# Kernel optimization log

Measured on AMD Instinct MI355X. Metric: run time of the kernel, lower is better.

Reference implementation:

```python
import jax, jax.numpy as jnp
from jax import lax
import numpy as np

INPUT_POINTS = 4096
NUM_STAGES = 4
EMBED_DIM = 72
K_NEIGHBORS = 90
ALPHA = 1000.0
BETA = 100.0
B = 4
EPS = 1e-5


def pos_embed(coords, out_dim):
    """coords: [B, Cin, *rest] -> [B, out_dim, *rest].
    Matches PosE_Initial/PosE_Geo: sin/cos interleaved along the feature axis."""
    Bsz, cin = coords.shape[0], coords.shape[1]
    rest = coords.shape[2:]
    feat_dim = out_dim // (cin * 2)
    dim_embed = ALPHA ** (jnp.arange(feat_dim, dtype=coords.dtype) / feat_dim)
    div = BETA * coords[..., None] / dim_embed                 # [B,Cin,*rest,f]
    emb = jnp.stack([jnp.sin(div), jnp.cos(div)], axis=-1)      # [B,Cin,*rest,f,2]
    emb = emb.reshape(coords.shape + (2 * feat_dim,))           # interleave sin/cos
    emb = jnp.moveaxis(emb, -1, 2)                              # [B,Cin,2f,*rest]
    return emb.reshape((Bsz, out_dim) + rest)


def fps(points, n):
    """Farthest point sampling, deterministic start at index 0. points [N,3]."""
    d0 = jnp.full(points.shape[0], jnp.inf, dtype=points.dtype)

    def step(carry, _):
        d, last = carry
        dist = jnp.sum((points - points[last]) ** 2, axis=-1)
        d = jnp.minimum(d, dist)
        return (d, jnp.argmax(d)), last

    _, idx = lax.scan(step, (d0, jnp.argmax(jnp.zeros(points.shape[0]))), None, length=n)
    return idx


def gather_points(points, idx):
    # points [B,N,C], idx [B,...] -> [B,...,C]
    return jax.vmap(lambda p, i: p[i])(points, idx)


def knn_indices(xyz, new_xyz, k):
    # squared pairwise distances [B,S,N] then k smallest
    sq = (jnp.sum(new_xyz ** 2, -1)[:, :, None]
          + jnp.sum(xyz ** 2, -1)[:, None, :]
          - 2.0 * jnp.einsum('bsc,bnc->bsn', new_xyz, xyz))
    _, idx = lax.top_k(-sq, k)
    return idx


def stage(xyz, x, group_num, out_dim, gamma, beta_p):
    # xyz [B,N,3], x [B,N,C]
    fi = fps(xyz[0], group_num)                 # shared across batch (fps with batch=None)
    lc_xyz = xyz[:, fi]                         # [B,G,3]
    lc_x = x[:, fi]                             # [B,G,C]
    ki = knn_indices(xyz, lc_xyz, K_NEIGHBORS)  # [B,G,K]
    knn_xyz = gather_points(xyz, ki)            # [B,G,K,3]
    knn_x = gather_points(x, ki)                # [B,G,K,C]
    # LGA: global scalar std (unbiased, like torch.std) normalization
    dx = knn_x - lc_x[:, :, None, :]
    dxyz = knn_xyz - lc_xyz[:, :, None, :]
    knn_xn = dx / (jnp.std(dx, ddof=1) + EPS)
    knn_xyzn = dxyz / (jnp.std(dxyz, ddof=1) + EPS)
    feat = jnp.concatenate(
        [knn_xn, jnp.broadcast_to(lc_x[:, :, None, :], knn_xn.shape)], axis=-1)
    feat = jnp.transpose(feat, (0, 3, 1, 2))                    # [B,out,G,K]
    pe = pos_embed(jnp.transpose(knn_xyzn, (0, 3, 1, 2)), out_dim)
    w = (feat + pe) * pe                                        # [B,out,G,K]
    # Pooling: max+mean over K, BatchNorm1d (training stats), exact GELU
    lc = jnp.max(w, -1) + jnp.mean(w, -1)                       # [B,out,G]
    mu = jnp.mean(lc, axis=(0, 2), keepdims=True)
    var = jnp.var(lc, axis=(0, 2), keepdims=True)
    lc = (lc - mu) / jnp.sqrt(var + EPS) * gamma[None, :, None] + beta_p[None, :, None]
    return lc_xyz, jax.nn.gelu(lc, approximate=False)


def forward(xyz, x, gammas, betas):
    feat = pos_embed(x, EMBED_DIM)              # [B,72,N]
    out_dim = EMBED_DIM
    group = INPUT_POINTS
    for i in range(NUM_STAGES):
        out_dim *= 2
        group //= 2
        xyz, feat = stage(xyz, jnp.transpose(feat, (0, 2, 1)),
                          group, out_dim, gammas[i], betas[i])
    return jnp.max(feat, -1) + jnp.mean(feat, -1)


def setup_inputs() -> dict:
    key = jax.random.key(0)
    k1, k2 = jax.random.split(key)
    inp = {
        'xyz': jax.random.normal(k1, (B, INPUT_POINTS, 3), jnp.float32),
        'x': jax.random.normal(k2, (B, 3, INPUT_POINTS), jnp.float32),
    }
    dims = [EMBED_DIM * 2 ** (i + 1) for i in range(NUM_STAGES)]
    for i, d in enumerate(dims):
        inp[f'gamma{i}'] = jnp.ones((d,), jnp.float32)
        inp[f'beta{i}'] = jnp.zeros((d,), jnp.float32)
    return inp


def reference(xyz, x, gamma0, beta0, gamma1, beta1, gamma2, beta2, gamma3, beta3):
    return forward(xyz, x,
                   [gamma0, gamma1, gamma2, gamma3],
                   [beta0, beta1, beta2, beta3])
```

## Files before the change

kernel.cpp:

```cpp
#include <hip/hip_runtime.h>

typedef unsigned int u32;
typedef unsigned long long u64;
typedef float v2f __attribute__((ext_vector_type(2)));

#define BB 4
#define NP0 4096
#define KNB 90
#define CC0 72
#define MAXD 1152
#define NSTRIPE 16
#define FSPLIT 850

__global__ void k_init(const float* __restrict__ xyz, const float* __restrict__ x,
                       float* __restrict__ xs, float* __restrict__ ys, float* __restrict__ zs,
                       float* __restrict__ feat, float* __restrict__ sums){
  int i = blockIdx.x*blockDim.x + threadIdx.x;
  if (i < 16) sums[i] = 0.f;
  if (i < BB*NP0){
    xs[i] = xyz[3*i+0];
    ys[i] = xyz[3*i+1];
    zs[i] = xyz[3*i+2];
  }
  if (i < BB*NP0*36){
    int j = i % 36; int bn = i / 36;
    int n = bn % NP0, b = bn / NP0;
    int cin = j / 12, f = j % 12;
    float xv = x[(b*3+cin)*NP0 + n];
    float rcp = __powf(1000.0f, -(float)f / 12.0f);
    float a = (100.0f * xv) * rcp;
    float sn, cs; __sincosf(a, &sn, &cs);
    float2 v = make_float2(sn, cs);
    *(float2*)(feat + (size_t)bn*CC0 + cin*24 + 2*f) = v;
  }
}

__device__ __forceinline__ void wave_argmax(float bd, int bi, float &smax, int &wbi){
  float v = bd;
  #define DPP_MAX(ctrl) do{ int _t = __builtin_amdgcn_mov_dpp(__float_as_int(v), (ctrl), 0xf, 0xf, true); \
                            v = fmaxf(v, __int_as_float(_t)); }while(0)
  DPP_MAX(0x111); DPP_MAX(0x112); DPP_MAX(0x114); DPP_MAX(0x118);
  DPP_MAX(0x142); DPP_MAX(0x143);
  #undef DPP_MAX
  smax = __int_as_float(__builtin_amdgcn_readlane(__float_as_int(v), 63));
  u64 msk = __ballot(bd == smax);
  int winlane = (int)__ffsll((long long)msk) - 1;
  wbi = __builtin_amdgcn_readlane(bi, winlane);
}

template<int PPT>
__global__ __launch_bounds__(256)
void k_fps4(const float* __restrict__ xs, const float* __restrict__ ys, const float* __restrict__ zs,
            int N, int G, int* __restrict__ fi,
            float* __restrict__ nxs, float* __restrict__ nys, float* __restrict__ nzs){
  constexpr int PH = PPT/2;
  __shared__ float4 sp[4096];
  __shared__ int sfi[2048];
  __shared__ u64 cand[2][4];
  int tid = threadIdx.x;
  const int base = tid * PPT;
  int wv = tid >> 6;
  int lane = tid & 63;
  v2f px[PH], py[PH], pz[PH], dmn[PH];
  #pragma unroll
  for (int j=0;j<PH;j++){
    int n = base + 2*j;
    float2 ax = *(const float2*)(xs+n);
    float2 ay = *(const float2*)(ys+n);
    float2 az = *(const float2*)(zs+n);
    px[j] = (v2f){ax.x, ax.y};
    py[j] = (v2f){ay.x, ay.y};
    pz[j] = (v2f){az.x, az.y};
    sp[n]   = make_float4(ax.x, ay.x, az.x, 0.f);
    sp[n+1] = make_float4(ax.y, ay.y, az.y, 0.f);
    dmn[j] = (v2f){INFINITY, INFINITY};
  }
  if (tid==0){ sfi[0]=0; }
  float lx = xs[0], ly = ys[0], lz = zs[0];
  __syncthreads();
  for (int t=1; t<G; t++){
    float bd = -INFINITY; int bi = base;
    v2f lx2 = (v2f){lx,lx}, ly2 = (v2f){ly,ly}, lz2 = (v2f){lz,lz};
    {
      #pragma clang fp contract(off)
      #pragma unroll
      for (int j=0;j<PH;j++){
        v2f dx = px[j] - lx2;
        v2f dy = py[j] - ly2;
        v2f dz = pz[j] - lz2;
        v2f d2 = (dx*dx + dy*dy) + dz*dz;
        v2f dmo = dmn[j];
        float dm0 = fminf(dmo.x, d2.x);
        float dm1 = fminf(dmo.y, d2.y);
        dmn[j] = (v2f){dm0, dm1};
        bool g0 = dm0 > bd;
        bd = g0 ? dm0 : bd;
        bi = g0 ? (base + 2*j) : bi;
        bool g1 = dm1 > bd;
        bd = g1 ? dm1 : bd;
        bi = g1 ? (base + 2*j + 1) : bi;
      }
    }
    float smax; int wbi;
    wave_argmax(bd, bi, smax, wbi);
    int par = t & 1;
    if (lane == 0) cand[par][wv] = ((u64)__float_as_uint(smax) << 32) | (u32)(~(u32)wbi);
    __syncthreads();
    u64 k0 = cand[par][0], k1 = cand[par][1], k2 = cand[par][2], k3 = cand[par][3];
    u64 ka = k0 > k1 ? k0 : k1;
    u64 kb = k2 > k3 ? k2 : k3;
    u64 km = ka > kb ? ka : kb;
    int w = (int)(~(u32)km);
    if ((u32)w >= (u32)N) w = 0;
    float4 p = sp[w];
    lx = p.x; ly = p.y; lz = p.z;
    if (tid==0){ sfi[t] = w; }
  }
  __syncthreads();
  for (int i = tid; i < G; i += 256) fi[i] = sfi[i];
  for (int i = tid; i < BB*G; i += 256){
    int b = i / G, g = i % G;
    int idx = sfi[g];
    nxs[i] = xs[(size_t)b*N + idx];
    nys[i] = ys[(size_t)b*N + idx];
    nzs[i] = zs[(size_t)b*N + idx];
  }
}

template<int NF, int NT, bool LDSST>
__device__ __forceinline__
void fps_chunk(const float* __restrict__ cxs, const float* __restrict__ cys, const float* __restrict__ czs,
               int t0, int t1,
               float* __restrict__ dmnG, float4* __restrict__ cenG,
               int* __restrict__ fi2,
               float* __restrict__ n2xs, float* __restrict__ n2ys, float* __restrict__ n2zs,
               u64 (&cand)[2][4], float4* __restrict__ sp){
  constexpr int PPT = NF/NT;
  constexpr int PH = PPT/2;
  constexpr int G2 = NF/2;
  constexpr int NW = NT/64;
  int tid = threadIdx.x;
  const int base = tid * PPT;
  int wv = tid >> 6, lane = tid & 63;
  v2f px[PH], py[PH], pz[PH], dmn[PH];
  #pragma unroll
  for (int j=0;j<PH;j++){
    int n = base + 2*j;
    float2 ax = *(const float2*)(cxs+n);
    float2 ay = *(const float2*)(cys+n);
    float2 az = *(const float2*)(czs+n);
    px[j] = (v2f){ax.x, ax.y};
    py[j] = (v2f){ay.x, ay.y};
    pz[j] = (v2f){az.x, az.y};
    if constexpr (LDSST){
      sp[n]   = make_float4(ax.x, ay.x, az.x, 0.f);
      sp[n+1] = make_float4(ax.y, ay.y, az.y, 0.f);
    }
  }
  float lx, ly, lz;
  if (t0 == 1){
    #pragma unroll
    for (int j=0;j<PH;j++) dmn[j] = (v2f){INFINITY, INFINITY};
    if (tid==0) fi2[0] = 0;
    lx = cxs[0]; ly = cys[0]; lz = czs[0];
  } else {
    #pragma unroll
    for (int j=0;j<PH;j++){
      float2 dv = *(const float2*)(dmnG + base + 2*j);
      dmn[j] = (v2f){dv.x, dv.y};
    }
    float4 c = *cenG;
    lx = c.x; ly = c.y; lz = c.z;
  }
  __syncthreads();
  for (int t=t0; t<t1; t++){
    float bd = -INFINITY; int bi = base;
    v2f lx2 = (v2f){lx,lx}, ly2 = (v2f){ly,ly}, lz2 = (v2f){lz,lz};
    {
      #pragma clang fp contract(off)
      #pragma unroll
      for (int j=0;j<PH;j++){
        v2f dx = px[j] - lx2;
        v2f dy = py[j] - ly2;
        v2f dz = pz[j] - lz2;
        v2f d2 = (dx*dx + dy*dy) + dz*dz;
        v2f dmo = dmn[j];
        float dm0 = fminf(dmo.x, d2.x);
        float dm1 = fminf(dmo.y, d2.y);
        dmn[j] = (v2f){dm0, dm1};
        bool g0 = dm0 > bd;
        bd = g0 ? dm0 : bd;
        bi = g0 ? (base + 2*j) : bi;
        bool g1 = dm1 > bd;
        bd = g1 ? dm1 : bd;
        bi = g1 ? (base + 2*j + 1) : bi;
      }
    }
    float smax; int wbi;
    wave_argmax(bd, bi, smax, wbi);
    int par = t & 1;
    if (lane == 0) cand[par][wv] = ((u64)__float_as_uint(smax) << 32) | (u32)(~(u32)wbi);
    __syncthreads();
    u64 km;
    if constexpr (NW >= 4){
      u64 k0 = cand[par][0], k1 = cand[par][1], k2 = cand[par][2], k3 = cand[par][3];
      u64 ka = k0 > k1 ? k0 : k1;
      u64 kb = k2 > k3 ? k2 : k3;
      km = ka > kb ? ka : kb;
    } else {
      u64 k0 = cand[par][0], k1 = cand[par][1];
      km = k0 > k1 ? k0 : k1;
    }
    int w = (int)(~(u32)km);
    if ((u32)w >= (u32)NF) w = 0;
    if constexpr (LDSST){
      float4 p = sp[w];
      lx = p.x; ly = p.y; lz = p.z;
    } else {
      lx = cxs[w]; ly = cys[w]; lz = czs[w];
    }
    if (tid==0) fi2[t] = w;
  }
  if (t1 < G2){
    #pragma unroll
    for (int j=0;j<PH;j++)
      *(float2*)(dmnG + base + 2*j) = make_float2(dmn[j].x, dmn[j].y);
    if (tid==0) *cenG = make_float4(lx, ly, lz, 0.f);
  } else {
    __syncthreads();
    for (int i = tid; i < BB*G2; i += NT){
      int b2 = i / G2, g2 = i % G2;
      int idx = fi2[g2];
      if ((u32)idx >= (u32)NF) idx = 0;
      n2xs[i] = cxs[(size_t)b2*NF + idx];
      n2ys[i] = cys[(size_t)b2*NF + idx];
      n2zs[i] = czs[(size_t)b2*NF + idx];
    }
  }
}

__device__ float blockReduceSum(float v, float* sRed){
  for (int off=32; off; off>>=1) v += __shfl_down(v, off, 64);
  int wid = threadIdx.x >> 6, lane = threadIdx.x & 63;
  __syncthreads();
  if (lane==0) sRed[wid] = v;
  __syncthreads();
  float r = 0;
  if (threadIdx.x == 0){ for (int i=0;i<4;i++) r += sRed[i]; }
  return r;
}

template<int C, int NF>
__global__ __launch_bounds__(256)
void k_knnstd(const float* __restrict__ x,
              const float* __restrict__ xs, const float* __restrict__ ys, const float* __restrict__ zs,
              const float* __restrict__ nxs, const float* __restrict__ nys, const float* __restrict__ nzs,
              const int* __restrict__ fi, int N, int G,
              int* __restrict__ ki, float* __restrict__ sums,
              int t0, int t1, float* __restrict__ dmnG, float4* __restrict__ cenG,
              int* __restrict__ fi2, float* __restrict__ n2xs,
              float* __restrict__ n2ys, float* __restrict__ n2zs){
  extern __shared__ u32 smk[];
  __shared__ u64 candF[2][4];
  int tid = threadIdx.x;
  if constexpr (NF > 0){
    if (blockIdx.x == 0){
      fps_chunk<NF,256,true>(nxs, nys, nzs, t0, t1, dmnG, cenG, fi2, n2xs, n2ys, n2zs, candF, (float4*)smk);
      return;
    }
  }
  u32* keys = smk;
  u32* hist = smk + N;
  u32* eq   = hist + 256;
  u32* sc   = eq + 512;
  u32* wtot = sc + 4;
  __shared__ float sLcx[C];
  __shared__ int sKi[KNB];
  __shared__ int sFi;
  __shared__ float sRed[4];
  int bid = (NF > 0) ? ((int)blockIdx.x - 1) : (int)blockIdx.x;
  int wv = tid >> 6, lane = tid & 63;
  int g = bid % G, b = bid / G;
  if (tid==0){ int f0 = fi[g]; if ((u32)f0 >= (u32)N) f0 = 0; sFi = f0; }
  float cx = nxs[b*G+g], cy = nys[b*G+g], cz = nzs[b*G+g];
  float ss = __fadd_rn(__fadd_rn(__fmul_rn(cx,cx), __fmul_rn(cy,cy)), __fmul_rn(cz,cz));
  for (int n = tid; n < N; n += 256){
    float px = xs[b*N+n], py = ys[b*N+n], pz = zs[b*N+n];
    float nn  = __fadd_rn(__fadd_rn(__fmul_rn(px,px), __fmul_rn(py,py)), __fmul_rn(pz,pz));
    float dot = __fadd_rn(__fadd_rn(__fmul_rn(cx,px), __fmul_rn(cy,py)), __fmul_rn(cz,pz));
    float sq  = __fsub_rn(__fadd_rn(ss, nn), __fmul_rn(2.0f, dot));
    u32 u = __float_as_uint(sq);
    keys[n] = (u & 0x80000000u) ? ~u : (u | 0x80000000u);
  }
  if (tid < 4) sc[tid] = 0;
  __syncthreads();
  for (int c = tid; c < C; c += 256) sLcx[c] = x[(size_t)(b*N + sFi)*C + c];
  u32 prefix = 0, bas = 0;
  for (int pass=0; pass<4; pass++){
    int shift = 24 - 8*pass;
    u32 mask = (pass==0) ? 0u : (0xFFFFFFFFu << (shift+8));
    hist[tid] = 0;
    __syncthreads();
    for (int n = tid; n < N; n += 256){
      u32 k = keys[n];
      if ((k & mask) == (prefix & mask))
        atomicAdd(&hist[(k >> shift) & 255u], 1u);
    }
    __syncthreads();
    u32 h = hist[tid];
    u32 p = h;
    #pragma unroll
    for (int off=1; off<64; off<<=1){
      u32 o = __shfl_up(p, off, 64);
      if (lane >= off) p += o;
    }
    if (lane == 63) wtot[wv] = p;
    __syncthreads();
    u32 ex = p - h;
    for (int w2=0; w2<wv; w2++) ex += wtot[w2];
    if (bas + ex < KNB && bas + ex + h >= KNB){
      sc[0] = prefix | ((u32)tid << shift);
      sc[1] = bas + ex;
    }
    __syncthreads();
    prefix = sc[0]; bas = sc[1];
    __syncthreads();
  }
  u32 T = prefix;
  int needEq = KNB - (int)bas;
  int* out = ki + (size_t)(b*G+g)*KNB;
  for (int n = tid; n < N; n += 256){
    u32 k = keys[n];
    if (k < T){
      u32 p2 = atomicAdd(&sc[2], 1u);
      if (p2 < KNB){ out[p2] = n; sKi[p2] = n; }
    } else if (k == T){
      u32 e = atomicAdd(&sc[3], 1u);
      if (e < 512) eq[e] = (u32)n;
    }
  }
  __syncthreads();
  int m = (int)sc[3]; if (m > 512) m = 512;
  for (int i = tid; i < m; i += 256){
    u32 v = eq[i];
    int r = 0;
    for (int j=0; j<m; j++) r += (eq[j] < v);
    if (r < needEq){
      u32 p2 = atomicAdd(&sc[2], 1u);
      if (p2 < KNB){ out[p2] = (int)v; sKi[p2] = (int)v; }
    }
  }
  __syncthreads();
  if (tid == 0){
    u32 c = sc[2];
    while (c < KNB){ out[c] = 0; sKi[c] = 0; c++; }
  }
  __syncthreads();
  float s1=0, s2=0, s3=0, s4=0;
  constexpr int C2 = C/2;
  for (int u2 = tid; u2 < KNB*C2; u2 += 256){
    int k = u2 / C2; int c = (u2 - k*C2)*2;
    int idx = sKi[k];
    float2 v = *(const float2*)(x + (size_t)(b*N + idx)*C + c);
    float a0 = v.x - sLcx[c];
    float a1 = v.y - sLcx[c+1];
    s1 += a0 + a1; s2 += a0*a0 + a1*a1;
  }
  if (tid < 3){
    for (int k=0;k<KNB;k++){
      int idx = sKi[k];
      float pc = (tid==0 ? xs[b*N+idx] : tid==1 ? ys[b*N+idx] : zs[b*N+idx]);
      float cc = (tid==0 ? cx : tid==1 ? cy : cz);
      float w = pc - cc;
      s3 += w; s4 += w*w;
    }
  }
  float t;
  t = blockReduceSum(s1, sRed); if (tid==0) atomicAdd(&sums[0], t);
  t = blockReduceSum(s2, sRed); if (tid==0) atomicAdd(&sums[1], t);
  t = blockReduceSum(s3, sRed); if (tid==0) atomicAdd(&sums[2], t);
  t = blockReduceSum(s4, sRed); if (tid==0) atomicAdd(&sums[3], t);
}

template<int C, int NF, int NT>
__global__ void k_feat(const float* __restrict__ x,
            const float* __restrict__ xs, const float* __restrict__ ys, const float* __restrict__ zs,
            const float* __restrict__ nxs, const float* __restrict__ nys, const float* __restrict__ nzs,
            const int* __restrict__ fi, const int* __restrict__ ki, const float* __restrict__ sums,
            double n1, double n2,
            int N, int G, float* __restrict__ lc,
            int t0, int t1, float* __restrict__ dmnG, float4* __restrict__ cenG,
            int* __restrict__ fi2, float* __restrict__ n2xs,
            float* __restrict__ n2ys, float* __restrict__ n2zs){
  constexpr int D = 2*C;
  constexpr int D3 = D/3;
  constexpr int FD = C/3;
  __shared__ u64 candF[2][4];
  __shared__ float sLcx[C];
  __shared__ float sDx[KNB*3];
  __shared__ int sKi[KNB];
  __shared__ int sFi;
  __shared__ float sC[3];
  __shared__ float sInv2[2];
  int tid = threadIdx.x;
  if constexpr (NF > 0){
    if (blockIdx.x == 0){
      fps_chunk<NF,NT,false>(nxs, nys, nzs, t0, t1, dmnG, cenG, fi2, n2xs, n2ys, n2zs, candF, nullptr);
      return;
    }
  }
  int bid = (NF > 0) ? ((int)blockIdx.x - 1) : (int)blockIdx.x;
  int g = bid % G, b = bid / G;
  if (tid==0){ int f0 = fi[g]; if ((u32)f0 >= (u32)N) f0 = 0; sFi = f0; }
  if (tid==0){
    double s1 = sums[0], s2 = sums[1];
    double mean = s1/n1;
    double var = (s2 - s1*mean)/(n1 - 1.0); if (var < 0) var = 0;
    sInv2[0] = (float)(1.0/(sqrt(var) + 1e-5));
    double t1d = sums[2], t2d = sums[3];
    double m2 = t1d/n2;
    double v2 = (t2d - t1d*m2)/(n2 - 1.0); if (v2 < 0) v2 = 0;
    sInv2[1] = (float)(1.0/(sqrt(v2) + 1e-5));
  }
  if (tid<3) sC[tid] = (tid==0 ? nxs[b*G+g] : tid==1 ? nys[b*G+g] : nzs[b*G+g]);
  if (tid < KNB){ int v = ki[(size_t)(b*G+g)*KNB + tid]; if ((u32)v >= (u32)N) v = 0; sKi[tid] = v; }
  __syncthreads();
  for (int c = tid; c < C; c += blockDim.x) sLcx[c] = x[(size_t)(b*N + sFi)*C + c];
  for (int t = tid; t < KNB*3; t += blockDim.x){
    int k = t/3, c = t%3;
    int idx = sKi[k];
    float pc = (c==0 ? xs[b*N+idx] : c==1 ? ys[b*N+idx] : zs[b*N+idx]);
    sDx[t] = (pc - sC[c]) * sInv2[1];
  }
  __syncthreads();
  int p = tid;
  if (p >= C) return;
  int d0 = 2*p;
  int c = d0 / D3;
  int f = (d0 - c*D3) >> 1;
  float rcp = __powf(1000.0f, -(float)f / (float)FD);
  bool low = (d0 < C);
  float invdx = sInv2[0];
  float fh0 = 0.f, fh1 = 0.f;
  if (!low){ fh0 = sLcx[d0-C]; fh1 = sLcx[d0+1-C]; }
  float l0 = low ? sLcx[d0] : 0.f, l1 = low ? sLcx[d0+1] : 0.f;
  float mx0=-INFINITY, mx1=-INFINITY, sm0=0.f, sm1=0.f;
  for (int k=0;k<KNB;k++){
    float a = (100.0f * sDx[k*3+c]) * rcp;
    float sn, cs; __sincosf(a, &sn, &cs);
    float f0, f1;
    if (low){
      float2 v = *(const float2*)(x + (size_t)(b*N + sKi[k])*C + d0);
      f0 = (v.x - l0) * invdx;
      f1 = (v.y - l1) * invdx;
    } else { f0 = fh0; f1 = fh1; }
    float w0 = (f0 + sn)*sn;
    float w1 = (f1 + cs)*cs;
    mx0 = fmaxf(mx0, w0); sm0 += w0;
    mx1 = fmaxf(mx1, w1); sm1 += w1;
  }
  float* o = lc + (size_t)(b*G+g)*D + d0;
  o[0] = mx0 + sm0/90.0f;
  o[1] = mx1 + sm1/90.0f;
}

__global__ __launch_bounds__(256)
void k_bnpart(const float* __restrict__ lc, int D, int M,
              double* __restrict__ PS, double* __restrict__ PQ){
  __shared__ double sS[4][64], sQ[4][64];
  int lane = threadIdx.x & 63, row = threadIdx.x >> 6;
  int tile = blockIdx.x, stripe = blockIdx.y;
  int d = tile*64 + lane;
  int span = M / NSTRIPE;
  int i0 = stripe * span;
  double s=0, q=0;
  if (d < D){
    for (int i=i0+row; i<i0+span; i+=4){
      float v = lc[(size_t)i*D + d];
      s += v; q += (double)v*v;
    }
  }
  sS[row][lane]=s; sQ[row][lane]=q;
  __syncthreads();
  if (row==0 && d < D){
    PS[(size_t)stripe*MAXD + d] = sS[0][lane]+sS[1][lane]+sS[2][lane]+sS[3][lane];
    PQ[(size_t)stripe*MAXD + d] = sQ[0][lane]+sQ[1][lane]+sQ[2][lane]+sQ[3][lane];
  }
}

__global__ void k_bnfin(const double* __restrict__ PS, const double* __restrict__ PQ,
                        const float* __restrict__ gamma, const float* __restrict__ beta,
                        int D, int M, float* __restrict__ A, float* __restrict__ Bb){
  int d = blockIdx.x*64 + threadIdx.x;
  if (d >= D) return;
  double ts=0, tq=0;
  for (int s=0; s<NSTRIPE; s++){ ts += PS[(size_t)s*MAXD + d]; tq += PQ[(size_t)s*MAXD + d]; }
  double mean = ts / M;
  double var = tq / M - mean*mean; if (var < 0) var = 0;
  float rstd = (float)(1.0/sqrt(var + 1e-5));
  float gm = gamma[d], bt = beta[d];
  A[d] = gm*rstd;
  Bb[d] = bt - (float)mean*gm*rstd;
}

__global__ void k_apply(float* __restrict__ lc, const float* __restrict__ A,
                        const float* __restrict__ Bb, int D, int total){
  int i = blockIdx.x*blockDim.x + threadIdx.x;
  if (i >= total) return;
  int d = i % D;
  float v = lc[i]*A[d] + Bb[d];
  lc[i] = 0.5f * v * (1.0f + erff(v * 0.70710678118654752f));
}

__global__ void k_out(const float* __restrict__ feat, float* __restrict__ out){
  int i = blockIdx.x*blockDim.x + threadIdx.x;
  if (i >= BB*1152) return;
  int b = i / 1152, d = i % 1152;
  const float* base = feat + (size_t)b*256*1152 + d;
  float mx = -INFINITY, sm = 0.f;
  for (int g=0; g<256; g++){
    float v = base[(size_t)g*1152];
    mx = fmaxf(mx, v); sm += v;
  }
  out[i] = mx + sm/256.0f;
}

extern "C" void kernel_launch(void* const* d_in, const int* in_sizes, int n_in,
                              void* d_out, int out_size, void* d_ws, size_t ws_size,
                              hipStream_t stream) {
  const float* xyz = (const float*)d_in[0];
  const float* xin = (const float*)d_in[1];
  float* ws = (float*)d_ws;
  size_t off = 0;
  const size_t PS_ = (size_t)BB*NP0;
  const size_t XS = (size_t)BB*NP0*CC0;
  float* T0[3]; float* T1[3]; float* T2[3];
  for (int i=0;i<3;i++){ T0[i] = ws + off; off += PS_; }
  for (int i=0;i<3;i++){ T1[i] = ws + off; off += PS_; }
  for (int i=0;i<3;i++){ T2[i] = ws + off; off += PS_; }
  float* xA = ws + off; off += XS;
  float* xB = ws + off; off += XS;
  int*   fiA = (int*)(ws + off); off += 2048;
  int*   fiB = (int*)(ws + off); off += 2048;
  int*   ki = (int*)(ws + off); off += (size_t)BB*2048*KNB;
  float* sums = ws + off; off += 16;
  float* Abn  = ws + off; off += 1152;
  float* Bbn  = ws + off; off += 1152;
  float* dmnG = ws + off; off += 2048;
  float4* cenG = (float4*)(ws + off); off += 4;
  off = (off + 1) & ~(size_t)1;
  double* PSb = (double*)(ws + off); off += (size_t)NSTRIPE*MAXD*2;
  double* PQb = (double*)(ws + off); off += (size_t)NSTRIPE*MAXD*2;

  k_init<<<(BB*NP0*36+255)/256, 256, 0, stream>>>(xyz, xin, T0[0], T0[1], T0[2], xA, sums);
  k_fps4<16><<<1, 256, 0, stream>>>(T0[0],T0[1],T0[2], NP0, NP0/2, fiA, T1[0],T1[1],T1[2]);

  float **P = T0, **Cn = T1, **Nx = T2;
  int *fiC = fiA, *fiN = fiB;
  float *xc = xA, *lc = xB;
  for (int s=0; s<4; s++){
    int N = NP0 >> s, G = N >> 1, C = CC0 << s, D = 2*C;
    float* ssum = sums + 4*s;
    size_t knn_need = (size_t)(N + 256 + 512 + 8 + 8)*4;
    if (s==0){
      size_t lds = knn_need; size_t fps_need = (size_t)2048*16;
      if (fps_need > lds) lds = fps_need;
      k_knnstd<72,2048><<<BB*G+1, 256, lds, stream>>>(xc, P[0],P[1],P[2], Cn[0],Cn[1],Cn[2],
          fiC, N, G, ki, ssum, 1, FSPLIT, dmnG, cenG, fiN, Nx[0],Nx[1],Nx[2]);
    } else if (s==1){
      size_t lds = knn_need; size_t fps_need = (size_t)1024*16;
      if (fps_need > lds) lds = fps_need;
      k_knnstd<144,1024><<<BB*G+1, 256, lds, stream>>>(xc, P[0],P[1],P[2], Cn[0],Cn[1],Cn[2],
          fiC, N, G, ki, ssum, 1, 512, dmnG, cenG, fiN, Nx[0],Nx[1],Nx[2]);
    } else if (s==2){
      size_t lds = knn_need; size_t fps_need = (size_t)512*16;
      if (fps_need > lds) lds = fps_need;
      k_knnstd<288,512><<<BB*G+1, 256, lds, stream>>>(xc, P[0],P[1],P[2], Cn[0],Cn[1],Cn[2],
          fiC, N, G, ki, ssum, 1, 256, dmnG, cenG, fiN, Nx[0],Nx[1],Nx[2]);
    } else {
      k_knnstd<576,0><<<BB*G, 256, knn_need, stream>>>(xc, P[0],P[1],P[2], Cn[0],Cn[1],Cn[2],
          fiC, N, G, ki, ssum, 0, 0, nullptr, nullptr, nullptr, nullptr, nullptr, nullptr);
    }
    double n1 = (double)BB*G*KNB*C, n2 = (double)BB*G*KNB*3;
    int Tp = ((C + 63)/64)*64;
    if (s==0){
      k_feat<72,2048,128><<<BB*G+1, Tp, 0, stream>>>(xc, P[0],P[1],P[2], Cn[0],Cn[1],Cn[2], fiC, ki, ssum,
          n1, n2, N, G, lc, FSPLIT, 1024, dmnG, cenG, fiN, Nx[0],Nx[1],Nx[2]);
    } else if (s==1){
      k_feat<144,0,0><<<BB*G, Tp, 0, stream>>>(xc, P[0],P[1],P[2], Cn[0],Cn[1],Cn[2], fiC, ki, ssum,
          n1, n2, N, G, lc, 0, 0, nullptr, nullptr, nullptr, nullptr, nullptr, nullptr);
    } else if (s==2){
      k_feat<288,0,0><<<BB*G, Tp, 0, stream>>>(xc, P[0],P[1],P[2], Cn[0],Cn[1],Cn[2], fiC, ki, ssum,
          n1, n2, N, G, lc, 0, 0, nullptr, nullptr, nullptr, nullptr, nullptr, nullptr);
    } else {
      k_feat<576,0,0><<<BB*G, Tp, 0, stream>>>(xc, P[0],P[1],P[2], Cn[0],Cn[1],Cn[2], fiC, ki, ssum,
          n1, n2, N, G, lc, 0, 0, nullptr, nullptr, nullptr, nullptr, nullptr, nullptr);
    }
    int M = BB*G;
    dim3 bng((D + 63)/64, NSTRIPE);
    k_bnpart<<<bng, 256, 0, stream>>>(lc, D, M, PSb, PQb);
    k_bnfin<<<(D + 63)/64, 64, 0, stream>>>(PSb, PQb, (const float*)d_in[2+2*s],
                                            (const float*)d_in[3+2*s], D, M, Abn, Bbn);
    int total = M*D;
    k_apply<<<(total+255)/256, 256, 0, stream>>>(lc, Abn, Bbn, D, total);
    float** t = P; P = Cn; Cn = Nx; Nx = t;
    int* ti = fiC; fiC = fiN; fiN = ti;
    float* tf = xc; xc = lc; lc = tf;
  }
  k_out<<<(BB*1152+255)/256, 256, 0, stream>>>(xc, (float*)d_out);
}
```

Baseline: 2.531 ms.

## Run FPS inside the KNN kernel and let KNN blocks spin on per-index flags

Result: no change. 2.572 ms (+1.6%).

```diff
diff --git a/kernel.cpp b/kernel.cpp
--- a/kernel.cpp
+++ b/kernel.cpp
@@ -10,13 +10,29 @@
 #define CC0 72
 #define MAXD 1152
 #define NSTRIPE 16
-#define FSPLIT 850
+#define T1S 300
+#define T2S 200
+
+__device__ __forceinline__ void fi_store(int* p, int v){
+  __hip_atomic_store(p, v, __ATOMIC_RELAXED, __HIP_MEMORY_SCOPE_AGENT);
+}
+__device__ __forceinline__ int fi_spin(const int* p){
+  int v = __hip_atomic_load((int*)p, __ATOMIC_RELAXED, __HIP_MEMORY_SCOPE_AGENT);
+  int guard = 0;
+  while (v == -1 && guard < (1<<20)){
+    __builtin_amdgcn_s_sleep(8);
+    v = __hip_atomic_load((int*)p, __ATOMIC_RELAXED, __HIP_MEMORY_SCOPE_AGENT);
+    guard++;
+  }
+  return v;
+}
 
 __global__ void k_init(const float* __restrict__ xyz, const float* __restrict__ x,
                        float* __restrict__ xs, float* __restrict__ ys, float* __restrict__ zs,
-                       float* __restrict__ feat, float* __restrict__ sums){
+                       float* __restrict__ feat, float* __restrict__ sums, int* __restrict__ fiALL){
   int i = blockIdx.x*blockDim.x + threadIdx.x;
   if (i < 16) sums[i] = 0.f;
+  if (i < 3840) fiALL[i] = -1;
   if (i < BB*NP0){
     xs[i] = xyz[3*i+0];
     ys[i] = xyz[3*i+1];
@@ -46,85 +62,6 @@
   u64 msk = __ballot(bd == smax);
   int winlane = (int)__ffsll((long long)msk) - 1;
   wbi = __builtin_amdgcn_readlane(bi, winlane);
-}
-
-template<int PPT>
-__global__ __launch_bounds__(256)
-void k_fps4(const float* __restrict__ xs, const float* __restrict__ ys, const float* __restrict__ zs,
-            int N, int G, int* __restrict__ fi,
-            float* __restrict__ nxs, float* __restrict__ nys, float* __restrict__ nzs){
-  constexpr int PH = PPT/2;
-  __shared__ float4 sp[4096];
-  __shared__ int sfi[2048];
-  __shared__ u64 cand[2][4];
-  int tid = threadIdx.x;
-  const int base = tid * PPT;
-  int wv = tid >> 6;
-  int lane = tid & 63;
-  v2f px[PH], py[PH], pz[PH], dmn[PH];
-  #pragma unroll
-  for (int j=0;j<PH;j++){
-    int n = base + 2*j;
-    float2 ax = *(const float2*)(xs+n);
-    float2 ay = *(const float2*)(ys+n);
-    float2 az = *(const float2*)(zs+n);
-    px[j] = (v2f){ax.x, ax.y};
-    py[j] = (v2f){ay.x, ay.y};
-    pz[j] = (v2f){az.x, az.y};
-    sp[n]   = make_float4(ax.x, ay.x, az.x, 0.f);
-    sp[n+1] = make_float4(ax.y, ay.y, az.y, 0.f);
-    dmn[j] = (v2f){INFINITY, INFINITY};
-  }
-  if (tid==0){ sfi[0]=0; }
-  float lx = xs[0], ly = ys[0], lz = zs[0];
-  __syncthreads();
-  for (int t=1; t<G; t++){
-    float bd = -INFINITY; int bi = base;
-    v2f lx2 = (v2f){lx,lx}, ly2 = (v2f){ly,ly}, lz2 = (v2f){lz,lz};
-    {
-      #pragma clang fp contract(off)
-      #pragma unroll
-      for (int j=0;j<PH;j++){
-        v2f dx = px[j] - lx2;
-        v2f dy = py[j] - ly2;
-        v2f dz = pz[j] - lz2;
-        v2f d2 = (dx*dx + dy*dy) + dz*dz;
-        v2f dmo = dmn[j];
-        float dm0 = fminf(dmo.x, d2.x);
-        float dm1 = fminf(dmo.y, d2.y);
-        dmn[j] = (v2f){dm0, dm1};
-        bool g0 = dm0 > bd;
-        bd = g0 ? dm0 : bd;
-        bi = g0 ? (base + 2*j) : bi;
-        bool g1 = dm1 > bd;
-        bd = g1 ? dm1 : bd;
-        bi = g1 ? (base + 2*j + 1) : bi;
-      }
-    }
-    float smax; int wbi;
-    wave_argmax(bd, bi, smax, wbi);
-    int par = t & 1;
-    if (lane == 0) cand[par][wv] = ((u64)__float_as_uint(smax) << 32) | (u32)(~(u32)wbi);
-    __syncthreads();
-    u64 k0 = cand[par][0], k1 = cand[par][1], k2 = cand[par][2], k3 = cand[par][3];
-    u64 ka = k0 > k1 ? k0 : k1;
-    u64 kb = k2 > k3 ? k2 : k3;
-    u64 km = ka > kb ? ka : kb;
-    int w = (int)(~(u32)km);
-    if ((u32)w >= (u32)N) w = 0;
-    float4 p = sp[w];
-    lx = p.x; ly = p.y; lz = p.z;
-    if (tid==0){ sfi[t] = w; }
-  }
-  __syncthreads();
-  for (int i = tid; i < G; i += 256) fi[i] = sfi[i];
-  for (int i = tid; i < BB*G; i += 256){
-    int b = i / G, g = i % G;
-    int idx = sfi[g];
-    nxs[i] = xs[(size_t)b*N + idx];
-    nys[i] = ys[(size_t)b*N + idx];
-    nzs[i] = zs[(size_t)b*N + idx];
-  }
 }
 
 template<int NF, int NT, bool LDSST>
@@ -140,95 +77,104 @@
   constexpr int G2 = NF/2;
   constexpr int NW = NT/64;
   int tid = threadIdx.x;
+  const bool act = (tid < NT);
   const int base = tid * PPT;
   int wv = tid >> 6, lane = tid & 63;
   v2f px[PH], py[PH], pz[PH], dmn[PH];
-  #pragma unroll
-  for (int j=0;j<PH;j++){
-    int n = base + 2*j;
-    float2 ax = *(const float2*)(cxs+n);
-    float2 ay = *(const float2*)(cys+n);
-    float2 az = *(const float2*)(czs+n);
-    px[j] = (v2f){ax.x, ax.y};
-    py[j] = (v2f){ay.x, ay.y};
-    pz[j] = (v2f){az.x, az.y};
-    if constexpr (LDSST){
-      sp[n]   = make_float4(ax.x, ay.x, az.x, 0.f);
-      sp[n+1] = make_float4(ax.y, ay.y, az.y, 0.f);
-    }
-  }
-  float lx, ly, lz;
-  if (t0 == 1){
-    #pragma unroll
-    for (int j=0;j<PH;j++) dmn[j] = (v2f){INFINITY, INFINITY};
-    if (tid==0) fi2[0] = 0;
-    lx = cxs[0]; ly = cys[0]; lz = czs[0];
-  } else {
+  float lx=0.f, ly=0.f, lz=0.f;
+  if (act){
     #pragma unroll
     for (int j=0;j<PH;j++){
-      float2 dv = *(const float2*)(dmnG + base + 2*j);
-      dmn[j] = (v2f){dv.x, dv.y};
-    }
-    float4 c = *cenG;
-    lx = c.x; ly = c.y; lz = c.z;
+      int n = base + 2*j;
+      float2 ax = *(const float2*)(cxs+n);
+      float2 ay = *(const float2*)(cys+n);
+      float2 az = *(const float2*)(czs+n);
+      px[j] = (v2f){ax.x, ax.y};
+      py[j] = (v2f){ay.x, ay.y};
+      pz[j] = (v2f){az.x, az.y};
+      if constexpr (LDSST){
+        sp[n]   = make_float4(ax.x, ay.x, az.x, 0.f);
+        sp[n+1] = make_float4(ax.y, ay.y, az.y, 0.f);
+      }
+    }
+    if (t0 == 1){
+      #pragma unroll
+      for (int j=0;j<PH;j++) dmn[j] = (v2f){INFINITY, INFINITY};
+      if (tid==0) fi_store(&fi2[0], 0);
+      lx = cxs[0]; ly = cys[0]; lz = czs[0];
+    } else {
+      #pragma unroll
+      for (int j=0;j<PH;j++){
+        float2 dv = *(const float2*)(dmnG + base + 2*j);
+        dmn[j] = (v2f){dv.x, dv.y};
+      }
+      float4 c = *cenG;
+      lx = c.x; ly = c.y; lz = c.z;
+    }
   }
   __syncthreads();
   for (int t=t0; t<t1; t++){
     float bd = -INFINITY; int bi = base;
-    v2f lx2 = (v2f){lx,lx}, ly2 = (v2f){ly,ly}, lz2 = (v2f){lz,lz};
-    {
-      #pragma clang fp contract(off)
+    float smax; int wbi;
+    if (act){
+      v2f lx2 = (v2f){lx,lx}, ly2 = (v2f){ly,ly}, lz2 = (v2f){lz,lz};
+      {
+        #pragma clang fp contract(off)
+        #pragma unroll
+        for (int j=0;j<PH;j++){
+          v2f dx = px[j] - lx2;
+          v2f dy = py[j] - ly2;
+          v2f dz = pz[j] - lz2;
+          v2f d2 = (dx*dx + dy*dy) + dz*dz;
+          v2f dmo = dmn[j];
+          float dm0 = fminf(dmo.x, d2.x);
+          float dm1 = fminf(dmo.y, d2.y);
+          dmn[j] = (v2f){dm0, dm1};
+          bool g0 = dm0 > bd;
+          bd = g0 ? dm0 : bd;
+          bi = g0 ? (base + 2*j) : bi;
+          bool g1 = dm1 > bd;
+          bd = g1 ? dm1 : bd;
+          bi = g1 ? (base + 2*j + 1) : bi;
+        }
+      }
+      wave_argmax(bd, bi, smax, wbi);
+      if (lane == 0) cand[t & 1][wv] = ((u64)__float_as_uint(smax) << 32) | (u32)(~(u32)wbi);
+    }
+    __syncthreads();
+    if (act){
+      int par = t & 1;
+      u64 km;
+      if constexpr (NW >= 4){
+        u64 k0 = cand[par][0], k1 = cand[par][1], k2 = cand[par][2], k3 = cand[par][3];
+        u64 ka = k0 > k1 ? k0 : k1;
+        u64 kb = k2 > k3 ? k2 : k3;
+        km = ka > kb ? ka : kb;
+      } else {
+        u64 k0 = cand[par][0], k1 = cand[par][1];
+        km = k0 > k1 ? k0 : k1;
+      }
+      int w = (int)(~(u32)km);
+      if ((u32)w >= (u32)NF) w = 0;
+      if constexpr (LDSST){
+        float4 p = sp[w];
+        lx = p.x; ly = p.y; lz = p.z;
+      } else {
+        lx = cxs[w]; ly = cys[w]; lz = czs[w];
+      }
+      if (tid==0) fi_store(&fi2[t], w);
+    }
+  }
+  if (t1 < G2){
+    if (act){
       #pragma unroll
-      for (int j=0;j<PH;j++){
-        v2f dx = px[j] - lx2;
-        v2f dy = py[j] - ly2;
-        v2f dz = pz[j] - lz2;
-        v2f d2 = (dx*dx + dy*dy) + dz*dz;
-        v2f dmo = dmn[j];
-        float dm0 = fminf(dmo.x, d2.x);
-        float dm1 = fminf(dmo.y, d2.y);
-        dmn[j] = (v2f){dm0, dm1};
-        bool g0 = dm0 > bd;
-        bd = g0 ? dm0 : bd;
-        bi = g0 ? (base + 2*j) : bi;
-        bool g1 = dm1 > bd;
-        bd = g1 ? dm1 : bd;
-        bi = g1 ? (base + 2*j + 1) : bi;
-      }
-    }
-    float smax; int wbi;
-    wave_argmax(bd, bi, smax, wbi);
-    int par = t & 1;
-    if (lane == 0) cand[par][wv] = ((u64)__float_as_uint(smax) << 32) | (u32)(~(u32)wbi);
-    __syncthreads();
-    u64 km;
-    if constexpr (NW >= 4){
-      u64 k0 = cand[par][0], k1 = cand[par][1], k2 = cand[par][2], k3 = cand[par][3];
-      u64 ka = k0 > k1 ? k0 : k1;
-      u64 kb = k2 > k3 ? k2 : k3;
-      km = ka > kb ? ka : kb;
-    } else {
-      u64 k0 = cand[par][0], k1 = cand[par][1];
-      km = k0 > k1 ? k0 : k1;
-    }
-    int w = (int)(~(u32)km);
-    if ((u32)w >= (u32)NF) w = 0;
-    if constexpr (LDSST){
-      float4 p = sp[w];
-      lx = p.x; ly = p.y; lz = p.z;
-    } else {
-      lx = cxs[w]; ly = cys[w]; lz = czs[w];
-    }
-    if (tid==0) fi2[t] = w;
-  }
-  if (t1 < G2){
-    #pragma unroll
-    for (int j=0;j<PH;j++)
-      *(float2*)(dmnG + base + 2*j) = make_float2(dmn[j].x, dmn[j].y);
-    if (tid==0) *cenG = make_float4(lx, ly, lz, 0.f);
+      for (int j=0;j<PH;j++)
+        *(float2*)(dmnG + base + 2*j) = make_float2(dmn[j].x, dmn[j].y);
+      if (tid==0) *cenG = make_float4(lx, ly, lz, 0.f);
+    }
   } else {
     __syncthreads();
-    for (int i = tid; i < BB*G2; i += NT){
+    for (int i = tid; i < BB*G2; i += blockDim.x){
       int b2 = i / G2, g2 = i % G2;
       int idx = fi2[g2];
       if ((u32)idx >= (u32)NF) idx = 0;
@@ -250,7 +196,7 @@
   return r;
 }
 
-template<int C, int NF>
+template<int C, int NF, bool SPIN>
 __global__ __launch_bounds__(256)
 void k_knnstd(const float* __restrict__ x,
               const float* __restrict__ xs, const float* __restrict__ ys, const float* __restrict__ zs,
@@ -265,7 +211,7 @@
   int tid = threadIdx.x;
   if constexpr (NF > 0){
     if (blockIdx.x == 0){
-      fps_chunk<NF,256,true>(nxs, nys, nzs, t0, t1, dmnG, cenG, fi2, n2xs, n2ys, n2zs, candF, (float4*)smk);
+      fps_chunk<NF,256,true>(xs, ys, zs, t0, t1, dmnG, cenG, fi2, n2xs, n2ys, n2zs, candF, (float4*)smk);
       return;
     }
   }
@@ -281,8 +227,18 @@
   int bid = (NF > 0) ? ((int)blockIdx.x - 1) : (int)blockIdx.x;
   int wv = tid >> 6, lane = tid & 63;
   int g = bid % G, b = bid / G;
-  if (tid==0){ int f0 = fi[g]; if ((u32)f0 >= (u32)N) f0 = 0; sFi = f0; }
-  float cx = nxs[b*G+g], cy = nys[b*G+g], cz = nzs[b*G+g];
+  if constexpr (SPIN){
+    if (tid==0){ int f0 = fi_spin(&fi[g]); if ((u32)f0 >= (u32)N) f0 = 0; sFi = f0; }
+    __syncthreads();
+  } else {
+    if (tid==0){ int f0 = fi[g]; if ((u32)f0 >= (u32)N) f0 = 0; sFi = f0; }
+  }
+  float cx, cy, cz;
+  if constexpr (SPIN){
+    cx = xs[(size_t)b*N + sFi]; cy = ys[(size_t)b*N + sFi]; cz = zs[(size_t)b*N + sFi];
+  } else {
+    cx = nxs[b*G+g]; cy = nys[b*G+g]; cz = nzs[b*G+g];
+  }
   float ss = __fadd_rn(__fadd_rn(__fmul_rn(cx,cx), __fmul_rn(cy,cy)), __fmul_rn(cz,cz));
   for (int n = tid; n < N; n += 256){
     float px = xs[b*N+n], py = ys[b*N+n], pz = zs[b*N+n];
@@ -534,14 +490,14 @@
   size_t off = 0;
   const size_t PS_ = (size_t)BB*NP0;
   const size_t XS = (size_t)BB*NP0*CC0;
-  float* T0[3]; float* T1[3]; float* T2[3];
-  for (int i=0;i<3;i++){ T0[i] = ws + off; off += PS_; }
-  for (int i=0;i<3;i++){ T1[i] = ws + off; off += PS_; }
-  for (int i=0;i<3;i++){ T2[i] = ws + off; off += PS_; }
+  float* TA[3]; float* TB[3]; float* TC[3];
+  for (int i=0;i<3;i++){ TA[i] = ws + off; off += PS_; }
+  for (int i=0;i<3;i++){ TB[i] = ws + off; off += PS_; }
+  for (int i=0;i<3;i++){ TC[i] = ws + off; off += PS_; }
   float* xA = ws + off; off += XS;
   float* xB = ws + off; off += XS;
-  int*   fiA = (int*)(ws + off); off += 2048;
-  int*   fiB = (int*)(ws + off); off += 2048;
+  int* fiALL = (int*)(ws + off); off += 3840;
+  int* fi0 = fiALL, *fi1 = fiALL+2048, *fi2p = fiALL+3072, *fi3 = fiALL+3584;
   int*   ki = (int*)(ws + off); off += (size_t)BB*2048*KNB;
   float* sums = ws + off; off += 16;
   float* Abn  = ws + off; off += 1152;
@@ -552,60 +508,61 @@
   double* PSb = (double*)(ws + off); off += (size_t)NSTRIPE*MAXD*2;
   double* PQb = (double*)(ws + off); off += (size_t)NSTRIPE*MAXD*2;
 
-  k_init<<<(BB*NP0*36+255)/256, 256, 0, stream>>>(xyz, xin, T0[0], T0[1], T0[2], xA, sums);
-  k_fps4<16><<<1, 256, 0, stream>>>(T0[0],T0[1],T0[2], NP0, NP0/2, fiA, T1[0],T1[1],T1[2]);
-
-  float **P = T0, **Cn = T1, **Nx = T2;
-  int *fiC = fiA, *fiN = fiB;
+  k_init<<<(BB*NP0*36+255)/256, 256, 0, stream>>>(xyz, xin, TA[0], TA[1], TA[2], xA, sums, fiALL);
+
   float *xc = xA, *lc = xB;
-  for (int s=0; s<4; s++){
-    int N = NP0 >> s, G = N >> 1, C = CC0 << s, D = 2*C;
-    float* ssum = sums + 4*s;
-    size_t knn_need = (size_t)(N + 256 + 512 + 8 + 8)*4;
-    if (s==0){
-      size_t lds = knn_need; size_t fps_need = (size_t)2048*16;
-      if (fps_need > lds) lds = fps_need;
-      k_knnstd<72,2048><<<BB*G+1, 256, lds, stream>>>(xc, P[0],P[1],P[2], Cn[0],Cn[1],Cn[2],
-          fiC, N, G, ki, ssum, 1, FSPLIT, dmnG, cenG, fiN, Nx[0],Nx[1],Nx[2]);
-    } else if (s==1){
-      size_t lds = knn_need; size_t fps_need = (size_t)1024*16;
-      if (fps_need > lds) lds = fps_need;
-      k_knnstd<144,1024><<<BB*G+1, 256, lds, stream>>>(xc, P[0],P[1],P[2], Cn[0],Cn[1],Cn[2],
-          fiC, N, G, ki, ssum, 1, 512, dmnG, cenG, fiN, Nx[0],Nx[1],Nx[2]);
-    } else if (s==2){
-      size_t lds = knn_need; size_t fps_need = (size_t)512*16;
-      if (fps_need > lds) lds = fps_need;
-      k_knnstd<288,512><<<BB*G+1, 256, lds, stream>>>(xc, P[0],P[1],P[2], Cn[0],Cn[1],Cn[2],
-          fiC, N, G, ki, ssum, 1, 256, dmnG, cenG, fiN, Nx[0],Nx[1],Nx[2]);
-    } else {
-      k_knnstd<576,0><<<BB*G, 256, knn_need, stream>>>(xc, P[0],P[1],P[2], Cn[0],Cn[1],Cn[2],
-          fiC, N, G, ki, ssum, 0, 0, nullptr, nullptr, nullptr, nullptr, nullptr, nullptr);
-    }
-    double n1 = (double)BB*G*KNB*C, n2 = (double)BB*G*KNB*3;
-    int Tp = ((C + 63)/64)*64;
-    if (s==0){
-      k_feat<72,2048,128><<<BB*G+1, Tp, 0, stream>>>(xc, P[0],P[1],P[2], Cn[0],Cn[1],Cn[2], fiC, ki, ssum,
-          n1, n2, N, G, lc, FSPLIT, 1024, dmnG, cenG, fiN, Nx[0],Nx[1],Nx[2]);
-    } else if (s==1){
-      k_feat<144,0,0><<<BB*G, Tp, 0, stream>>>(xc, P[0],P[1],P[2], Cn[0],Cn[1],Cn[2], fiC, ki, ssum,
-          n1, n2, N, G, lc, 0, 0, nullptr, nullptr, nullptr, nullptr, nullptr, nullptr);
-    } else if (s==2){
-      k_feat<288,0,0><<<BB*G, Tp, 0, stream>>>(xc, P[0],P[1],P[2], Cn[0],Cn[1],Cn[2], fiC, ki, ssum,
-          n1, n2, N, G, lc, 0, 0, nullptr, nullptr, nullptr, nullptr, nullptr, nullptr);
-    } else {
-      k_feat<576,0,0><<<BB*G, Tp, 0, stream>>>(xc, P[0],P[1],P[2], Cn[0],Cn[1],Cn[2], fiC, ki, ssum,
-          n1, n2, N, G, lc, 0, 0, nullptr, nullptr, nullptr, nullptr, nullptr, nullptr);
-    }
-    int M = BB*G;
+  {
+    int N = 4096, G = 2048, D = 144;
+    k_knnstd<72,4096,true><<<BB*G+1, 256, 65536, stream>>>(xc, TA[0],TA[1],TA[2], TB[0],TB[1],TB[2],
+        fi0, N, G, ki, sums+0, 1, 2048, dmnG, cenG, fi0, TB[0],TB[1],TB[2]);
+    double n1 = (double)BB*G*KNB*72, n2 = (double)BB*G*KNB*3;
+    k_feat<72,2048,128><<<BB*G+1, 128, 0, stream>>>(xc, TA[0],TA[1],TA[2], TB[0],TB[1],TB[2], fi0, ki, sums+0,
+        n1, n2, N, G, lc, 1, T1S, dmnG, cenG, fi1, TC[0],TC[1],TC[2]);
     dim3 bng((D + 63)/64, NSTRIPE);
-    k_bnpart<<<bng, 256, 0, stream>>>(lc, D, M, PSb, PQb);
-    k_bnfin<<<(D + 63)/64, 64, 0, stream>>>(PSb, PQb, (const float*)d_in[2+2*s],
-                                            (const float*)d_in[3+2*s], D, M, Abn, Bbn);
-    int total = M*D;
-    k_apply<<<(total+255)/256, 256, 0, stream>>>(lc, Abn, Bbn, D, total);
-    float** t = P; P = Cn; Cn = Nx; Nx = t;
-    int* ti = fiC; fiC = fiN; fiN = ti;
-    float* tf = xc; xc = lc; lc = tf;
+    k_bnpart<<<bng, 256, 0, stream>>>(lc, D, BB*G, PSb, PQb);
+    k_bnfin<<<(D + 63)/64, 64, 0, stream>>>(PSb, PQb, (const float*)d_in[2], (const float*)d_in[3], D, BB*G, Abn, Bbn);
+    k_apply<<<(BB*G*D+255)/256, 256, 0, stream>>>(lc, Abn, Bbn, D, BB*G*D);
+    float* t = xc; xc = lc; lc = t;
+  }
+  {
+    int N = 2048, G = 1024, D = 288;
+    k_knnstd<144,2048,true><<<BB*G+1, 256, 32768, stream>>>(xc, TB[0],TB[1],TB[2], TC[0],TC[1],TC[2],
+        fi1, N, G, ki, sums+4, T1S, 1024, dmnG, cenG, fi1, TC[0],TC[1],TC[2]);
+    double n1 = (double)BB*G*KNB*144, n2 = (double)BB*G*KNB*3;
+    k_feat<144,1024,128><<<BB*G+1, 192, 0, stream>>>(xc, TB[0],TB[1],TB[2], TC[0],TC[1],TC[2], fi1, ki, sums+4,
+        n1, n2, N, G, lc, 1, T2S, dmnG, cenG, fi2p, TA[0],TA[1],TA[2]);
+    dim3 bng((D + 63)/64, NSTRIPE);
+    k_bnpart<<<bng, 256, 0, stream>>>(lc, D, BB*G, PSb, PQb);
+    k_bnfin<<<(D + 63)/64, 64, 0, stream>>>(PSb, PQb, (const float*)d_in[4], (const float*)d_in[5], D, BB*G, Abn, Bbn);
+    k_apply<<<(BB*G*D+255)/256, 256, 0, stream>>>(lc, Abn, Bbn, D, BB*G*D);
+    float* t = xc; xc = lc; lc = t;
+  }
+  {
+    int N = 1024, G = 512, D = 576;
+    k_knnstd<288,1024,true><<<BB*G+1, 256, 16384, stream>>>(xc, TC[0],TC[1],TC[2], TA[0],TA[1],TA[2],
+        fi2p, N, G, ki, sums+8, T2S, 512, dmnG, cenG, fi2p, TA[0],TA[1],TA[2]);
+    double n1 = (double)BB*G*KNB*288, n2 = (double)BB*G*KNB*3;
+    k_feat<288,512,256><<<BB*G+1, 320, 0, stream>>>(xc, TC[0],TC[1],TC[2], TA[0],TA[1],TA[2], fi2p, ki, sums+8,
+        n1, n2, N, G, lc, 1, 256, dmnG, cenG, fi3, TB[0],TB[1],TB[2]);
+    dim3 bng((D + 63)/64, NSTRIPE);
+    k_bnpart<<<bng, 256, 0, stream>>>(lc, D, BB*G, PSb, PQb);
+    k_bnfin<<<(D + 63)/64, 64, 0, stream>>>(PSb, PQb, (const float*)d_in[6], (const float*)d_in[7], D, BB*G, Abn, Bbn);
+    k_apply<<<(BB*G*D+255)/256, 256, 0, stream>>>(lc, Abn, Bbn, D, BB*G*D);
+    float* t = xc; xc = lc; lc = t;
+  }
+  {
+    int N = 512, G = 256, D = 1152;
+    size_t knn_lds = (size_t)(N + 256 + 512 + 8 + 8)*4;
+    k_knnstd<576,0,false><<<BB*G, 256, knn_lds, stream>>>(xc, TA[0],TA[1],TA[2], TB[0],TB[1],TB[2],
+        fi3, N, G, ki, sums+12, 0, 0, nullptr, nullptr, nullptr, nullptr, nullptr, nullptr);
+    double n1 = (double)BB*G*KNB*576, n2 = (double)BB*G*KNB*3;
+    k_feat<576,0,0><<<BB*G, 576, 0, stream>>>(xc, TA[0],TA[1],TA[2], TB[0],TB[1],TB[2], fi3, ki, sums+12,
+        n1, n2, N, G, lc, 0, 0, nullptr, nullptr, nullptr, nullptr, nullptr, nullptr);
+    dim3 bng((D + 63)/64, NSTRIPE);
+    k_bnpart<<<bng, 256, 0, stream>>>(lc, D, BB*G, PSb, PQb);
+    k_bnfin<<<(D + 63)/64, 64, 0, stream>>>(PSb, PQb, (const float*)d_in[8], (const float*)d_in[9], D, BB*G, Abn, Bbn);
+    k_apply<<<(BB*G*D+255)/256, 256, 0, stream>>>(lc, Abn, Bbn, D, BB*G*D);
+    float* t = xc; xc = lc; lc = t;
   }
   k_out<<<(BB*1152+255)/256, 256, 0, stream>>>(xc, (float*)d_out);
 }
```
